# Performance work log

Hardware: AMD Instinct MI355X
Metric: run time of the kernel (lower is better)

Reference implementation:

```python
import jax, jax.numpy as jnp
import numpy as np

NUM_HEADS = 16
HEAD_DIM = 64  # d_out // num_heads


def setup_inputs() -> dict:
    key = jax.random.key(0)
    ks = jax.random.split(key, 6)
    d_in, d_out, b, t = 1024, 1024, 2, 2048
    s = 0.02
    return {
        "x": jax.random.normal(ks[0], (b, t, d_in), jnp.float32),
        "Wq": jax.random.normal(ks[1], (d_in, d_out), jnp.float32) * s,
        "Wk": jax.random.normal(ks[2], (d_in, d_out), jnp.float32) * s,
        "Wv": jax.random.normal(ks[3], (d_in, d_out), jnp.float32) * s,
        "Wo": jax.random.normal(ks[4], (d_out, d_out), jnp.float32) * s,
        "bo": jnp.zeros((d_out,), jnp.float32),
    }


def reference(x, Wq, Wk, Wv, Wo, bo):
    b, t, _ = x.shape
    H, hd = NUM_HEADS, HEAD_DIM
    # qkv projections (no bias), split into heads: [b, H, t, hd]
    q = (x @ Wq).reshape(b, t, H, hd).transpose(0, 2, 1, 3)
    k = (x @ Wk).reshape(b, t, H, hd).transpose(0, 2, 1, 3)
    v = (x @ Wv).reshape(b, t, H, hd).transpose(0, 2, 1, 3)
    # raw scores, causal mask (masked_fill with -1e9 BEFORE the 1/sqrt(hd) scale,
    # matching the source exactly), then scaled softmax
    scores = jnp.einsum("bhqd,bhkd->bhqk", q, k)
    causal = jnp.triu(jnp.ones((t, t), dtype=bool), k=1)
    scores = jnp.where(causal[None, None], jnp.float32(-1e9), scores)
    attn = jax.nn.softmax(scores / jnp.sqrt(jnp.float32(hd)), axis=-1)
    # dropout is identity in eval mode
    ctx = jnp.einsum("bhqk,bhkd->bhqd", attn, v)  # [b, H, t, hd]
    ctx = ctx.transpose(0, 2, 1, 3).reshape(b, t, H * hd)
    return ctx @ Wo + bo
```

## Files before the change

kernel.cpp:

```cpp
#include <hip/hip_runtime.h>


#define SEQ   2048
#define DMODEL 1024
#define NH    16
#define HD    64
#define MROWS 4096

typedef __attribute__((ext_vector_type(4))) float f32x4;
typedef __attribute__((ext_vector_type(16))) float f32x16;
typedef __attribute__((ext_vector_type(8))) short short8;
typedef __attribute__((ext_vector_type(4))) unsigned int u32x4;

#define MFMA16(a, b, c) __builtin_amdgcn_mfma_f32_16x16x32_bf16((a), (b), (c), 0, 0, 0)
#define MFMA32(a, b, c) __builtin_amdgcn_mfma_f32_32x32x16_bf16((a), (b), (c), 0, 0, 0)

__device__ __forceinline__ unsigned short f2bf(float f) {
  union { float f; unsigned u; } v; v.f = f;
  return (unsigned short)((v.u + 0x7fffu + ((v.u >> 16) & 1u)) >> 16);
}

__device__ __forceinline__ float exp2x(float x) {
#if __has_builtin(__builtin_amdgcn_exp2f)
  return __builtin_amdgcn_exp2f(x);
#else
  float r; asm("v_exp_f32 %0, %1" : "=v"(r) : "v"(x)); return r;
#endif
}

__device__ __forceinline__ unsigned cvt_pk(float lo, float hi) {
  unsigned r;
  asm volatile("v_cvt_pk_bf16_f32 %0, %1, %2" : "=v"(r) : "v"(lo), "v"(hi));
  return r;
}

__device__ __forceinline__ void pls(unsigned& a, unsigned& b) {
  asm("v_permlane32_swap_b32 %0, %1" : "+v"(a), "+v"(b));
}

__device__ __forceinline__ short8 as_short8(u32x4 v) {
  union { u32x4 u; short8 s; } x; x.u = v; return x.s;
}

__device__ __forceinline__ f32x4 zero4() {
  f32x4 z; z[0] = 0.f; z[1] = 0.f; z[2] = 0.f; z[3] = 0.f; return z;
}

__device__ __forceinline__ void async16(const void* g, void* l) {
  __builtin_amdgcn_global_load_lds(
      (const __attribute__((address_space(1))) unsigned int*)g,
      (__attribute__((address_space(3))) unsigned int*)l, 16, 0, 0);
}

__global__ __launch_bounds__(256) void xconv(const float* __restrict__ x,
                                             unsigned short* __restrict__ xb) {
  int i = blockIdx.x * 256 + threadIdx.x;
  const float4* p = (const float4*)x;
  float4 a = p[2 * i];
  float4 b = p[2 * i + 1];
  short8 o;
  o[0] = (short)f2bf(a.x); o[1] = (short)f2bf(a.y);
  o[2] = (short)f2bf(a.z); o[3] = (short)f2bf(a.w);
  o[4] = (short)f2bf(b.x); o[5] = (short)f2bf(b.y);
  o[6] = (short)f2bf(b.z); o[7] = (short)f2bf(b.w);
  *(short8*)&xb[(size_t)i * 8] = o;
}

__global__ __launch_bounds__(256) void wtrans(const float* __restrict__ W,
                                              unsigned short* __restrict__ Wt) {
  __shared__ unsigned short tile[64][65];
  int t = threadIdx.x;
  int tx = t & 63, ty = t >> 6;
  int kb = blockIdx.x * 64, nb = blockIdx.y * 64;
#pragma unroll
  for (int rr = 0; rr < 16; rr++) {
    int r = ty * 16 + rr;
    tile[r][tx] = f2bf(W[(size_t)(kb + r) * 1024 + nb + tx]);
  }
  __syncthreads();
#pragma unroll
  for (int rr = 0; rr < 16; rr++) {
    int r = ty * 16 + rr;
    Wt[(size_t)(nb + r) * 1024 + kb + tx] = tile[tx][r];
  }
}

__global__ __launch_bounds__(256) void vtrans(const unsigned short* __restrict__ V,
                                              unsigned short* __restrict__ Vt) {
  __shared__ unsigned short tile[64][65];
  int t = threadIdx.x;
  int tx = t & 63, ty = t >> 6;
  int bh = blockIdx.x, t0 = blockIdx.y * 64;
  const unsigned short* src = V + ((size_t)bh * SEQ + t0) * HD;
  unsigned short* dst = Vt + (size_t)bh * HD * SEQ + t0;
#pragma unroll
  for (int rr = 0; rr < 16; rr++) {
    int r = ty * 16 + rr;
    tile[r][tx] = src[(size_t)r * HD + tx];
  }
  __syncthreads();
#pragma unroll
  for (int rr = 0; rr < 16; rr++) {
    int r = ty * 16 + rr;
    dst[(size_t)r * SEQ + tx] = tile[tx][r];
  }
}

template <int MODE, int WMF>
__global__ __launch_bounds__(256) void gemm_bt(
    const unsigned short* __restrict__ A, const unsigned short* __restrict__ Bt,
    unsigned short* __restrict__ Qo, unsigned short* __restrict__ Ko,
    unsigned short* __restrict__ Vo, float* __restrict__ out,
    const float* __restrict__ bo) {
  constexpr int K = 1024;
  constexpr int BM = WMF * 32;
  constexpr int NT = K / 32;
  __shared__ __align__(16) unsigned short As[3][BM * 32];
  __shared__ __align__(16) unsigned short Bs[3][128 * 32];
  const int t = threadIdx.x;
  const int lane = t & 63;
  const int w = t >> 6;
  const int lr = lane & 15, kf = lane >> 4;
  const int wr = w >> 1, wc = w & 1;

  const int nwg = gridDim.x * gridDim.y;
  const int id = blockIdx.y * gridDim.x + blockIdx.x;
  const int swz = (id & 7) * (nwg >> 3) + (id >> 3);
  const int bx = swz % gridDim.x, by = swz / gridDim.x;

  const int rowbase = bx * BM;
  const int colbase = by * 128;

  const unsigned short* Ab = A + (size_t)rowbase * K;
  const unsigned short* Bb = Bt + (size_t)colbase * K;

  f32x4 acc[WMF][4];
#pragma unroll
  for (int m = 0; m < WMF; m++)
#pragma unroll
    for (int n = 0; n < 4; n++) acc[m][n] = zero4();

  auto stage = [&](int buf, int kt) {
    int k0 = kt * 32;
#pragma unroll
    for (int i = 0; i < BM / 64; i++) {
      int f = i * 256 + t;
      int c = f ^ ((f >> 3) & 3);
      int row = c >> 2;
      int col = (c & 3) << 3;
      async16(Ab + (size_t)row * K + k0 + col, (char*)&As[buf][0] + (size_t)f * 16);
    }
#pragma unroll
    for (int i = 0; i < 2; i++) {
      int f = i * 256 + t;
      int c = f ^ ((f >> 3) & 3);
      int row = c >> 2;
      int col = (c & 3) << 3;
      async16(Bb + (size_t)row * K + k0 + col, (char*)&Bs[buf][0] + (size_t)f * 16);
    }
  };

  stage(0, 0);
  stage(1, 1);

  for (int kt = 0; kt < NT; kt++) {
    if (kt + 2 < NT) {
      stage((kt + 2) % 3, kt + 2);
      if constexpr (MODE == 0) asm volatile("s_waitcnt vmcnt(8)" ::: "memory");
      else                     asm volatile("s_waitcnt vmcnt(6)" ::: "memory");
    } else if (kt + 1 < NT) {
      if constexpr (MODE == 0) asm volatile("s_waitcnt vmcnt(4)" ::: "memory");
      else                     asm volatile("s_waitcnt vmcnt(3)" ::: "memory");
    } else {
      asm volatile("s_waitcnt vmcnt(0)" ::: "memory");
    }
    __builtin_amdgcn_s_barrier();

    const int cur = kt % 3;
    short8 av[WMF], bv[4];
#pragma unroll
    for (int m = 0; m < WMF; m++) {
      int row = wr * (WMF * 16) + m * 16 + lr;
      int idx = (row * 32 + kf * 8) ^ (((row >> 1) & 3) << 3);
      av[m] = *(const short8*)&As[cur][idx];
    }
#pragma unroll
    for (int n = 0; n < 4; n++) {
      int row = wc * 64 + n * 16 + lr;
      int idx = (row * 32 + kf * 8) ^ (((row >> 1) & 3) << 3);
      bv[n] = *(const short8*)&Bs[cur][idx];
    }
    __builtin_amdgcn_s_setprio(1);
#pragma unroll
    for (int m = 0; m < WMF; m++)
#pragma unroll
      for (int n = 0; n < 4; n++) acc[m][n] = MFMA16(av[m], bv[n], acc[m][n]);
    __builtin_amdgcn_s_setprio(0);
    __builtin_amdgcn_s_barrier();
  }

  if constexpr (MODE == 0) {
#pragma unroll
    for (int n = 0; n < 4; n++) {
      int c = colbase + wc * 64 + n * 16 + lr;
      int sel = c >> 10;
      int hh = (c >> 6) & 15;
      int dd = c & 63;
      unsigned short* dst = (sel == 0) ? Qo : ((sel == 1) ? Ko : Vo);
      const float sc = (sel == 0) ? 0.18033688011112042f : 1.0f;
#pragma unroll
      for (int m = 0; m < WMF; m++) {
        int r0 = rowbase + wr * (WMF * 16) + m * 16 + kf * 4;
#pragma unroll
        for (int i = 0; i < 4; i++) {
          int r = r0 + i;
          int bi = r >> 11;
          int tq = r & 2047;
          size_t off = ((size_t)(bi * NH + hh) * SEQ + tq) * HD + dd;
          dst[off] = f2bf(acc[m][n][i] * sc);
        }
      }
    }
  } else {
#pragma unroll
    for (int n = 0; n < 4; n++) {
      int c = colbase + wc * 64 + n * 16 + lr;
      float bias = bo[c];
#pragma unroll
      for (int m = 0; m < WMF; m++) {
        int r0 = rowbase + wr * (WMF * 16) + m * 16 + kf * 4;
#pragma unroll
        for (int i = 0; i < 4; i++) {
          out[(size_t)(r0 + i) * 1024 + c] = acc[m][n][i] + bias;
        }
      }
    }
  }
}

__global__ __launch_bounds__(256) void attn_fwd(
    const unsigned short* __restrict__ Q, const unsigned short* __restrict__ K,
    const unsigned short* __restrict__ Vt, unsigned short* __restrict__ ctx) {
  const int bh = blockIdx.x;
  const int y = blockIdx.y;
  const int qt = (y < 8) ? (15 - y) : (y - 8);
  const int bi = bh >> 4, hh = bh & 15;
  const int t = threadIdx.x, lane = t & 63, w = t >> 6;
  const int qc = lane & 31, hi = lane >> 5;

  __shared__ __align__(16) unsigned short Ks[2][2][64 * 64];
  __shared__ __align__(16) unsigned short Vs[2][2][64 * 64];

  const unsigned short* Qb = Q + (size_t)bh * SEQ * HD;
  const unsigned short* Kb = K + (size_t)bh * SEQ * HD;
  const unsigned short* Vb = Vt + (size_t)bh * HD * SEQ;

  const int qrow = qt * 128 + w * 32;
  short8 qv[4];
#pragma unroll
  for (int c = 0; c < 4; c++)
    qv[c] = *(const short8*)&Qb[(size_t)(qrow + qc) * HD + c * 16 + hi * 8];

  f32x16 o0, o1;
#pragma unroll
  for (int i = 0; i < 16; i++) { o0[i] = 0.f; o1[i] = 0.f; }
  float l_acc = 0.f;

  const int ktmax = 2 * qt + (w >> 1);
  const int NP = qt + 1;

  auto stage = [&](int buf, int p) {
#pragma unroll
    for (int sub = 0; sub < 2; sub++) {
      int kt = 2 * p + sub;
#pragma unroll
      for (int i2 = 0; i2 < 2; i2++) {
        int f = i2 * 256 + t;
        int c = f ^ ((f >> 3) & 7);
        async16(Kb + (size_t)kt * 64 * HD + (size_t)c * 8,
                (char*)&Ks[buf][sub][0] + (size_t)f * 16);
        int d = c >> 3, ko = (c & 7) << 3;
        async16(Vb + (size_t)d * SEQ + (size_t)kt * 64 + ko,
                (char*)&Vs[buf][sub][0] + (size_t)f * 16);
      }
    }
  };

  auto tile = [&](const unsigned short* Kt, const unsigned short* Vtile, int kt) {
    f32x16 s0, s1;
#pragma unroll
    for (int i = 0; i < 16; i++) { s0[i] = 0.f; s1[i] = 0.f; }
    __builtin_amdgcn_s_setprio(1);
#pragma unroll
    for (int c = 0; c < 4; c++) {
      int i0 = (qc * 64 + c * 16 + hi * 8) ^ ((qc & 7) << 3);
      s0 = MFMA32(*(const short8*)&Kt[i0], qv[c], s0);
      int r1 = 32 + qc;
      int i1 = (r1 * 64 + c * 16 + hi * 8) ^ ((r1 & 7) << 3);
      s1 = MFMA32(*(const short8*)&Kt[i1], qv[c], s1);
    }
    __builtin_amdgcn_s_setprio(0);

    if (kt == ktmax) {
      const int qg = qrow + qc;
#pragma unroll
      for (int reg = 0; reg < 16; reg++) {
        int rloc = (reg & 3) + 8 * (reg >> 2) + 4 * hi;
        int kg = kt * 64 + rloc;
        if (kg > qg) s0[reg] = -1e30f;
        if (kg + 32 > qg) s1[reg] = -1e30f;
      }
    }

    unsigned w0[8], w1[8];
    float psA = 0.f, psB = 0.f;
#pragma unroll
    for (int j = 0; j < 8; j++) {
      float a0 = exp2x(s0[2 * j]), b0 = exp2x(s0[2 * j + 1]);
      float a1 = exp2x(s1[2 * j]), b1 = exp2x(s1[2 * j + 1]);
      psA += a0 + b0;
      psB += a1 + b1;
      w0[j] = cvt_pk(a0, b0);
      w1[j] = cvt_pk(a1, b1);
    }
    l_acc += psA + psB;

    __builtin_amdgcn_s_setprio(1);
#pragma unroll
    for (int h2 = 0; h2 < 2; h2++) {
      unsigned* pw = h2 ? w1 : w0;
#pragma unroll
      for (int cc = 0; cc < 2; cc++) {
        unsigned a0 = pw[cc * 4 + 0], b0 = pw[cc * 4 + 2];
        unsigned a1 = pw[cc * 4 + 1], b1 = pw[cc * 4 + 3];
        pls(a0, b0);
        pls(a1, b1);
        u32x4 pf; pf[0] = a0; pf[1] = a1; pf[2] = b0; pf[3] = b1;
        short8 pfrag = as_short8(pf);
        int c2 = h2 * 2 + cc;
        int ia = (qc * 64 + c2 * 16 + hi * 8) ^ ((qc & 7) << 3);
        o0 = MFMA32(*(const short8*)&Vtile[ia], pfrag, o0);
        int rb = 32 + qc;
        int ib = (rb * 64 + c2 * 16 + hi * 8) ^ ((rb & 7) << 3);
        o1 = MFMA32(*(const short8*)&Vtile[ib], pfrag, o1);
      }
    }
    __builtin_amdgcn_s_setprio(0);
  };

  stage(0, 0);
  int cur = 0;

  for (int p = 0; p < NP; p++) {
    if (p + 1 < NP) {
      stage(cur ^ 1, p + 1);
      asm volatile("s_waitcnt vmcnt(8)" ::: "memory");
    } else {
      asm volatile("s_waitcnt vmcnt(0)" ::: "memory");
    }
    __builtin_amdgcn_s_barrier();

    if (2 * p <= ktmax)     tile(&Ks[cur][0][0], &Vs[cur][0][0], 2 * p);
    if (2 * p + 1 <= ktmax) tile(&Ks[cur][1][0], &Vs[cur][1][0], 2 * p + 1);

    __builtin_amdgcn_s_barrier();
    cur ^= 1;
  }

  float l = l_acc + __shfl_xor(l_acc, 32);
  float inv = 1.0f / l;
  const size_t rowoff = ((size_t)bi * SEQ + qrow + qc) * DMODEL + hh * HD;
#pragma unroll
  for (int g = 0; g < 4; g++) {
    unsigned pa = cvt_pk(o0[4 * g] * inv, o0[4 * g + 1] * inv);
    unsigned pb = cvt_pk(o0[4 * g + 2] * inv, o0[4 * g + 3] * inv);
    uint2 vv; vv.x = pa; vv.y = pb;
    *(uint2*)&ctx[rowoff + 8 * g + 4 * hi] = vv;
    unsigned pc = cvt_pk(o1[4 * g] * inv, o1[4 * g + 1] * inv);
    unsigned pd = cvt_pk(o1[4 * g + 2] * inv, o1[4 * g + 3] * inv);
    uint2 ww; ww.x = pc; ww.y = pd;
    *(uint2*)&ctx[rowoff + 32 + 8 * g + 4 * hi] = ww;
  }
}

extern "C" void kernel_launch(void* const* d_in, const int* in_sizes, int n_in,
                              void* d_out, int out_size, void* d_ws, size_t ws_size,
                              hipStream_t stream) {
  const float* x  = (const float*)d_in[0];
  const float* Wq = (const float*)d_in[1];
  const float* Wk = (const float*)d_in[2];
  const float* Wv = (const float*)d_in[3];
  const float* Wo = (const float*)d_in[4];
  const float* bo = (const float*)d_in[5];
  float* out = (float*)d_out;

  unsigned short* xb   = (unsigned short*)d_ws;
  unsigned short* Wt   = xb + (size_t)MROWS * DMODEL;
  unsigned short* WoT  = Wt + (size_t)3 * 1024 * 1024;
  unsigned short* Qb   = WoT + (size_t)1024 * 1024;
  unsigned short* Kb   = Qb + (size_t)MROWS * DMODEL;
  unsigned short* Vb   = Kb + (size_t)MROWS * DMODEL;
  unsigned short* ctxb = Vb + (size_t)MROWS * DMODEL;

  xconv<<<2048, 256, 0, stream>>>(x, xb);
  dim3 tg(16, 16);
  wtrans<<<tg, 256, 0, stream>>>(Wq, Wt);
  wtrans<<<tg, 256, 0, stream>>>(Wk, Wt + (size_t)1024 * 1024);
  wtrans<<<tg, 256, 0, stream>>>(Wv, Wt + (size_t)2 * 1024 * 1024);
  wtrans<<<tg, 256, 0, stream>>>(Wo, WoT);

  gemm_bt<0, 4><<<dim3(32, 24), 256, 0, stream>>>(xb, Wt, Qb, Kb, ctxb, nullptr, nullptr);
  vtrans<<<dim3(32, 32), 256, 0, stream>>>(ctxb, Vb);
  attn_fwd<<<dim3(32, 16), 256, 0, stream>>>(Qb, Kb, Vb, ctxb);
  gemm_bt<1, 2><<<dim3(64, 8), 256, 0, stream>>>(ctxb, WoT, nullptr, nullptr, nullptr, out, bo);
}
```

Measured before the change: 121.1 us.

## Split attention blocks into 64-row query tiles with 2 waves each

Each attention block now handles a 64-row query tile with two waves instead of a 128-row tile with four, and the grid doubles to 32x32 blocks. Key/value staging now uses one 64-key tile per double buffer, with blocks ordered longest-first. This aims for finer load balance across the causal triangle, more resident blocks and less shared memory per block. In exchange, K/V tiles are reloaded by twice as many blocks and each block has fewer waves to hide latency.

```diff
diff --git a/kernel.cpp b/kernel.cpp
--- a/kernel.cpp
+++ b/kernel.cpp
@@ -238,24 +238,24 @@
   }
 }
 
-__global__ __launch_bounds__(256) void attn_fwd(
+__global__ __launch_bounds__(128) void attn_fwd(
     const unsigned short* __restrict__ Q, const unsigned short* __restrict__ K,
     const unsigned short* __restrict__ Vt, unsigned short* __restrict__ ctx) {
   const int bh = blockIdx.x;
-  const int y = blockIdx.y;
-  const int qt = (y < 8) ? (15 - y) : (y - 8);
+  const int qb = 31 - blockIdx.y;
   const int bi = bh >> 4, hh = bh & 15;
-  const int t = threadIdx.x, lane = t & 63, w = t >> 6;
+  const int t = threadIdx.x, w = t >> 6;
+  const int lane = t & 63;
   const int qc = lane & 31, hi = lane >> 5;
 
-  __shared__ __align__(16) unsigned short Ks[2][2][64 * 64];
-  __shared__ __align__(16) unsigned short Vs[2][2][64 * 64];
+  __shared__ __align__(16) unsigned short Ks[2][64 * 64];
+  __shared__ __align__(16) unsigned short Vs[2][64 * 64];
 
   const unsigned short* Qb = Q + (size_t)bh * SEQ * HD;
   const unsigned short* Kb = K + (size_t)bh * SEQ * HD;
   const unsigned short* Vb = Vt + (size_t)bh * HD * SEQ;
 
-  const int qrow = qt * 128 + w * 32;
+  const int qrow = qb * 64 + w * 32;
   short8 qv[4];
 #pragma unroll
   for (int c = 0; c < 4; c++)
@@ -266,23 +266,18 @@
   for (int i = 0; i < 16; i++) { o0[i] = 0.f; o1[i] = 0.f; }
   float l_acc = 0.f;
 
-  const int ktmax = 2 * qt + (w >> 1);
-  const int NP = qt + 1;
-
-  auto stage = [&](int buf, int p) {
-#pragma unroll
-    for (int sub = 0; sub < 2; sub++) {
-      int kt = 2 * p + sub;
-#pragma unroll
-      for (int i2 = 0; i2 < 2; i2++) {
-        int f = i2 * 256 + t;
-        int c = f ^ ((f >> 3) & 7);
-        async16(Kb + (size_t)kt * 64 * HD + (size_t)c * 8,
-                (char*)&Ks[buf][sub][0] + (size_t)f * 16);
-        int d = c >> 3, ko = (c & 7) << 3;
-        async16(Vb + (size_t)d * SEQ + (size_t)kt * 64 + ko,
-                (char*)&Vs[buf][sub][0] + (size_t)f * 16);
-      }
+  const int ktmax = qb;
+
+  auto stage = [&](int buf, int kt) {
+#pragma unroll
+    for (int i2 = 0; i2 < 4; i2++) {
+      int f = i2 * 128 + t;
+      int c = f ^ ((f >> 3) & 7);
+      async16(Kb + (size_t)kt * 64 * HD + (size_t)c * 8,
+              (char*)&Ks[buf][0] + (size_t)f * 16);
+      int d = c >> 3, ko = (c & 7) << 3;
+      async16(Vb + (size_t)d * SEQ + (size_t)kt * 64 + ko,
+              (char*)&Vs[buf][0] + (size_t)f * 16);
     }
   };
 
@@ -349,22 +344,19 @@
   };
 
   stage(0, 0);
-  int cur = 0;
-
-  for (int p = 0; p < NP; p++) {
-    if (p + 1 < NP) {
-      stage(cur ^ 1, p + 1);
+
+  for (int kt = 0; kt <= ktmax; kt++) {
+    if (kt < ktmax) {
+      stage((kt + 1) & 1, kt + 1);
       asm volatile("s_waitcnt vmcnt(8)" ::: "memory");
     } else {
       asm volatile("s_waitcnt vmcnt(0)" ::: "memory");
     }
     __builtin_amdgcn_s_barrier();
 
-    if (2 * p <= ktmax)     tile(&Ks[cur][0][0], &Vs[cur][0][0], 2 * p);
-    if (2 * p + 1 <= ktmax) tile(&Ks[cur][1][0], &Vs[cur][1][0], 2 * p + 1);
+    tile(&Ks[kt & 1][0], &Vs[kt & 1][0], kt);
 
     __builtin_amdgcn_s_barrier();
-    cur ^= 1;
   }
 
   float l = l_acc + __shfl_xor(l_acc, 32);
@@ -411,6 +403,6 @@
 
   gemm_bt<0, 4><<<dim3(32, 24), 256, 0, stream>>>(xb, Wt, Qb, Kb, ctxb, nullptr, nullptr);
   vtrans<<<dim3(32, 32), 256, 0, stream>>>(ctxb, Vb);
-  attn_fwd<<<dim3(32, 16), 256, 0, stream>>>(Qb, Kb, Vb, ctxb);
+  attn_fwd<<<dim3(32, 32), 128, 0, stream>>>(Qb, Kb, Vb, ctxb);
   gemm_bt<1, 2><<<dim3(64, 8), 256, 0, stream>>>(ctxb, WoT, nullptr, nullptr, nullptr, out, bo);
 }
```

After: 126.6 us. +4.5%, slower.

## Load K/V fragments directly into registers instead of staging through LDS

Applied to the files above, without the earlier changes.

Removes the shared-memory double buffer and block barriers from the attention kernel. Each wave now loads its K and V MFMA fragments straight from global memory into registers, double-buffered across two register sets with vmcnt waits. Each wave iterates only up to its own causal limit. This drops LDS traffic and synchronisation, but each of the four waves now fetches the same K/V tiles independently, raising global/L2 traffic and register pressure; launch bounds are also set to request 2 blocks per CU.

```diff
diff --git a/kernel.cpp b/kernel.cpp
--- a/kernel.cpp
+++ b/kernel.cpp
@@ -238,7 +238,7 @@
   }
 }
 
-__global__ __launch_bounds__(256) void attn_fwd(
+__global__ __launch_bounds__(256, 2) void attn_fwd(
     const unsigned short* __restrict__ Q, const unsigned short* __restrict__ K,
     const unsigned short* __restrict__ Vt, unsigned short* __restrict__ ctx) {
   const int bh = blockIdx.x;
@@ -248,9 +248,6 @@
   const int t = threadIdx.x, lane = t & 63, w = t >> 6;
   const int qc = lane & 31, hi = lane >> 5;
 
-  __shared__ __align__(16) unsigned short Ks[2][2][64 * 64];
-  __shared__ __align__(16) unsigned short Vs[2][2][64 * 64];
-
   const unsigned short* Qb = Q + (size_t)bh * SEQ * HD;
   const unsigned short* Kb = K + (size_t)bh * SEQ * HD;
   const unsigned short* Vb = Vt + (size_t)bh * HD * SEQ;
@@ -267,37 +264,30 @@
   float l_acc = 0.f;
 
   const int ktmax = 2 * qt + (w >> 1);
-  const int NP = qt + 1;
-
-  auto stage = [&](int buf, int p) {
-#pragma unroll
-    for (int sub = 0; sub < 2; sub++) {
-      int kt = 2 * p + sub;
-#pragma unroll
-      for (int i2 = 0; i2 < 2; i2++) {
-        int f = i2 * 256 + t;
-        int c = f ^ ((f >> 3) & 7);
-        async16(Kb + (size_t)kt * 64 * HD + (size_t)c * 8,
-                (char*)&Ks[buf][sub][0] + (size_t)f * 16);
-        int d = c >> 3, ko = (c & 7) << 3;
-        async16(Vb + (size_t)d * SEQ + (size_t)kt * 64 + ko,
-                (char*)&Vs[buf][sub][0] + (size_t)f * 16);
-      }
+
+  short8 kA[8], vA[8], kB[8], vB[8];
+
+  auto loadKV = [&](short8* kf, short8* vf, int kt) {
+    const unsigned short* Kt = Kb + (size_t)kt * 64 * HD;
+    const unsigned short* Vp = Vb + (size_t)kt * 64;
+#pragma unroll
+    for (int c = 0; c < 4; c++) {
+      kf[c]     = *(const short8*)&Kt[qc * 64 + c * 16 + hi * 8];
+      kf[4 + c] = *(const short8*)&Kt[(32 + qc) * 64 + c * 16 + hi * 8];
+      vf[c]     = *(const short8*)&Vp[(size_t)qc * SEQ + c * 16 + hi * 8];
+      vf[4 + c] = *(const short8*)&Vp[(size_t)(32 + qc) * SEQ + c * 16 + hi * 8];
     }
   };
 
-  auto tile = [&](const unsigned short* Kt, const unsigned short* Vtile, int kt) {
+  auto tilec = [&](const short8* kf, const short8* vf, int kt) {
     f32x16 s0, s1;
 #pragma unroll
     for (int i = 0; i < 16; i++) { s0[i] = 0.f; s1[i] = 0.f; }
     __builtin_amdgcn_s_setprio(1);
 #pragma unroll
     for (int c = 0; c < 4; c++) {
-      int i0 = (qc * 64 + c * 16 + hi * 8) ^ ((qc & 7) << 3);
-      s0 = MFMA32(*(const short8*)&Kt[i0], qv[c], s0);
-      int r1 = 32 + qc;
-      int i1 = (r1 * 64 + c * 16 + hi * 8) ^ ((r1 & 7) << 3);
-      s1 = MFMA32(*(const short8*)&Kt[i1], qv[c], s1);
+      s0 = MFMA32(kf[c], qv[c], s0);
+      s1 = MFMA32(kf[4 + c], qv[c], s1);
     }
     __builtin_amdgcn_s_setprio(0);
 
@@ -338,33 +328,34 @@
         u32x4 pf; pf[0] = a0; pf[1] = a1; pf[2] = b0; pf[3] = b1;
         short8 pfrag = as_short8(pf);
         int c2 = h2 * 2 + cc;
-        int ia = (qc * 64 + c2 * 16 + hi * 8) ^ ((qc & 7) << 3);
-        o0 = MFMA32(*(const short8*)&Vtile[ia], pfrag, o0);
-        int rb = 32 + qc;
-        int ib = (rb * 64 + c2 * 16 + hi * 8) ^ ((rb & 7) << 3);
-        o1 = MFMA32(*(const short8*)&Vtile[ib], pfrag, o1);
+        o0 = MFMA32(vf[c2], pfrag, o0);
+        o1 = MFMA32(vf[4 + c2], pfrag, o1);
       }
     }
     __builtin_amdgcn_s_setprio(0);
   };
 
-  stage(0, 0);
-  int cur = 0;
-
-  for (int p = 0; p < NP; p++) {
-    if (p + 1 < NP) {
-      stage(cur ^ 1, p + 1);
-      asm volatile("s_waitcnt vmcnt(8)" ::: "memory");
+  loadKV(kA, vA, 0);
+
+  int kt = 0;
+  for (;;) {
+    if (kt + 1 <= ktmax) {
+      loadKV(kB, vB, kt + 1);
+      asm volatile("s_waitcnt vmcnt(16)" ::: "memory");
     } else {
       asm volatile("s_waitcnt vmcnt(0)" ::: "memory");
     }
-    __builtin_amdgcn_s_barrier();
-
-    if (2 * p <= ktmax)     tile(&Ks[cur][0][0], &Vs[cur][0][0], 2 * p);
-    if (2 * p + 1 <= ktmax) tile(&Ks[cur][1][0], &Vs[cur][1][0], 2 * p + 1);
-
-    __builtin_amdgcn_s_barrier();
-    cur ^= 1;
+    tilec(kA, vA, kt);
+    if (++kt > ktmax) break;
+
+    if (kt + 1 <= ktmax) {
+      loadKV(kA, vA, kt + 1);
+      asm volatile("s_waitcnt vmcnt(16)" ::: "memory");
+    } else {
+      asm volatile("s_waitcnt vmcnt(0)" ::: "memory");
+    }
+    tilec(kB, vB, kt);
+    if (++kt > ktmax) break;
   }
 
   float l = l_acc + __shfl_xor(l_acc, 32);
```

Result: slower. 146.9 us (+21.3%).
